# Optimization experiments

Measured on AMD Instinct MI355X. Metric: run time of the kernel, lower is better.

Reference implementation:

```python
import jax, jax.numpy as jnp
import numpy as np

H = W = 224
NSR = NSC = 8          # num_segments_row / col
BW = 5                 # band_width (default of adjust_boundaries)
K = NSR * NSC          # 64 superpixels
B = 256


def find_paths(g, inits, bw):
    """Seam-carving DP along axis 0 of g. g: (L, M); inits: (P,) start columns.
    Returns optimal paths (P, L) of column indices per row."""
    L, M = g.shape
    P = inits.shape[0]
    idx_pos = jnp.clip(inits[:, None] + jnp.arange(-bw, bw + 1)[None, :], 0, M - 1)  # (P, Np)
    Np = idx_pos.shape[1]
    C = -g[:, idx_pos]  # (L, P, Np) unary cost per row
    neigh = jnp.clip(jnp.arange(Np)[:, None] + jnp.array([-1, 0, 1])[None, :], 0, Np - 1)  # (Np,3)
    pos = jnp.arange(Np)
    r = jnp.arange(P)

    def step(cost_prev, c_y):
        padded = jnp.pad(cost_prev, ((0, 0), (1, 1)), constant_values=jnp.inf)  # (P, Np+2)
        prev_costs = padded[:, neigh + 1]                                        # (P, Np, 3)
        min_prev = prev_costs.min(axis=-1)
        min_idx = prev_costs.argmin(axis=-1)          # first-min, matches torch .min
        path_y = neigh[pos[None, :], min_idx]          # (P, Np) backpointers
        return min_prev + c_y, path_y

    cost_last, path_arr = jax.lax.scan(step, C[0], C[1:])  # path_arr: (L-1, P, Np)
    idx = jnp.argmin(cost_last, axis=1)                    # (P,)

    def back(idx, p_y):
        out = idx_pos[r, idx]
        return p_y[r, idx], out

    idx0, outs = jax.lax.scan(back, idx, path_arr, reverse=True)  # outs: (L-1, P) for y=1..L-1
    out0 = idx_pos[r, idx0]
    paths = jnp.concatenate([out0[None], outs], axis=0)  # (L, P)
    return paths.T


def segment_image(g):
    """g: (H, W) gradient map -> (H, W) int32 segmentation labels."""
    x_inits = jnp.clip(jnp.arange(1, NSC) * (W // NSC), 0, W - 1)
    y_inits = jnp.clip(jnp.arange(1, NSR) * (H // NSR), 0, H - 1)
    vpaths = find_paths(g, x_inits, BW)      # (7, H): column index per row
    hpaths = find_paths(g.T, y_inits, BW)    # (7, W): row index per column
    rows = jnp.broadcast_to(jnp.arange(H), vpaths.shape)
    cols = jnp.broadcast_to(jnp.arange(W), hpaths.shape)
    vmask = jnp.zeros((H, W), jnp.int32).at[rows, vpaths].set(1)
    hmask = jnp.zeros((H, W), jnp.int32).at[hpaths, cols].set(1)
    vlab = jnp.cumsum(vmask, axis=1)   # vertical label in [0, 7]
    hlab = jnp.cumsum(hmask, axis=0)   # horizontal label in [0, 7]
    return vlab + NSC * hlab           # labels in [0, 63]


def centroids_of(mask):
    flat = mask.reshape(-1)
    yc = jnp.repeat(jnp.arange(H, dtype=jnp.float32), W)
    xc = jnp.tile(jnp.arange(W, dtype=jnp.float32), H)
    sy = jax.ops.segment_sum(yc, flat, num_segments=K)
    sx = jax.ops.segment_sum(xc, flat, num_segments=K)
    cnt = jnp.maximum(jax.ops.segment_sum(jnp.ones_like(yc), flat, num_segments=K), 1e-6)
    return jnp.stack([sy / cnt, sx / cnt], axis=-1)  # (K, 2) [y, x]


def setup_inputs() -> dict:
    key = jax.random.key(0)
    k1, k2 = jax.random.split(key)
    x = jax.random.normal(k1, (B, 3, H, W), dtype=jnp.float32)
    grad_map = jax.random.uniform(k2, (B, H, W), dtype=jnp.float32)
    return {"x": x, "grad_map": grad_map}


def reference(x, grad_map):
    masks = jax.vmap(segment_image)(grad_map)          # (B, H, W) int32
    cents = jax.vmap(centroids_of)(masks)              # (B, K, 2) float32
    return cents, masks.astype(jnp.int64)
```

## Files before the change

kernel.cpp:

```cpp
#include <hip/hip_runtime.h>
#include <stdint.h>

#define HH 224
#define WW 224
#define NSEAM 7
#define BWIDTH 5
#define BB 256
#define KK 64
#define YCH 8
#define YROWS (HH / YCH)

#define DPPF_OLD(old, src, ctrl) \
    __int_as_float(__builtin_amdgcn_update_dpp(__float_as_int(old), __float_as_int(src), ctrl, 0xF, 0xF, false))
#define DPPF_Z(src, ctrl) \
    __int_as_float(__builtin_amdgcn_update_dpp(0, __float_as_int(src), ctrl, 0xF, 0xF, true))
#define DPPI_Z(src, ctrl) \
    __builtin_amdgcn_update_dpp(0, (int)(src), ctrl, 0xF, 0xF, true)

__global__ __launch_bounds__(256) void dp_kernel(const float* __restrict__ g,
                                                 int* __restrict__ paths,
                                                 unsigned long long* __restrict__ gacc) {
    __shared__ uint32_t ch[16][226];
    __shared__ int      pth[16][226];

    {
        int t = blockIdx.x * 256 + threadIdx.x;
        if (t < BB * KK) gacc[t] = 0ull;
    }

    const int j   = threadIdx.x & 15;
    const int grp = threadIdx.x >> 4;
    const int gid = blockIdx.x * 16 + grp;
    const int dir = gid / (BB * NSEAM);
    const int rem = gid - dir * (BB * NSEAM);
    const int b   = rem / NSEAM;
    const int p   = rem - b * NSEAM;
    const int band0 = 28 * (p + 1) - BWIDTH;
    const int jc  = (j > 10) ? 10 : j;
    const float* gb  = g + (size_t)b * HH * WW;
    const float* gp0 = gb + band0 + jc;
    const float* gp1 = gb + (size_t)(band0 + jc) * WW;
    const int shb  = threadIdx.x & 48;
    const int sel0 = (j == 0) ? 1 : 0;

    float bufA[16], bufB[16], cost;

#define LOADC(BUF, c)                                                       \
    if (dir == 0) {                                                         \
        _Pragma("unroll")                                                   \
        for (int rr = 0; rr < 16; ++rr) BUF[rr] = gp0[((c) * 16 + rr) * WW];\
    } else {                                                                \
        const float4* q4 = reinterpret_cast<const float4*>(gp1 + (c) * 16); \
        float4 t0 = q4[0], t1 = q4[1], t2 = q4[2], t3 = q4[3];              \
        BUF[0] = t0.x;  BUF[1] = t0.y;  BUF[2] = t0.z;  BUF[3] = t0.w;      \
        BUF[4] = t1.x;  BUF[5] = t1.y;  BUF[6] = t1.z;  BUF[7] = t1.w;      \
        BUF[8] = t2.x;  BUF[9] = t2.y;  BUF[10] = t2.z; BUF[11] = t2.w;     \
        BUF[12] = t3.x; BUF[13] = t3.y; BUF[14] = t3.z; BUF[15] = t3.w;     \
    }

#define ROWSTEP(BUF, rr, rbase)                                             \
    {                                                                       \
        float pm  = DPPF_OLD(cost, cost, 0x111);   \
        float ppv = DPPF_OLD(cost, cost, 0x101);  \
        ppv = (j >= 10) ? cost : ppv;                            \
        float best = fminf(fminf(pm, cost), ppv);                           \
        int sel = (pm == best) ? sel0 : ((cost == best) ? 1 : 2);           \
        cost = best - BUF[rr];                                              \
        unsigned long long b0 = __ballot(sel & 1);                          \
        unsigned long long b1 = __ballot(sel & 2);                          \
        if (j == 0) ch[grp][(rbase) + rr] =                                 \
            (uint32_t)(((b0 >> shb) & 0xFFFFull) |                          \
                       (((b1 >> shb) & 0xFFFFull) << 16));                  \
    }

#define PROCC(BUF, cbase)                                                   \
    _Pragma("unroll")                                                       \
    for (int rr = 0; rr < 16; ++rr) ROWSTEP(BUF, rr, (cbase) * 16)

    LOADC(bufA, 0);
    LOADC(bufB, 1);
    cost = -bufA[0];
#pragma unroll
    for (int rr = 1; rr < 16; ++rr) ROWSTEP(bufA, rr, 0);
    LOADC(bufA, 2);
    PROCC(bufB, 1);
    LOADC(bufB, 3);

#pragma unroll 1
    for (int c2 = 2; c2 <= 12; c2 += 2) {
        PROCC(bufA, c2);
        if (c2 + 2 < 14) LOADC(bufA, c2 + 2);
        PROCC(bufB, c2 + 1);
        if (c2 + 3 < 14) LOADC(bufB, c2 + 3);
    }

    float rc = (j <= 10) ? cost : INFINITY;
    int   ri = (j <= 10) ? j : 15;
#define REDSTEP(ctrl)                                                        \
    {                                                                        \
        float oc = DPPF_Z(rc, ctrl);                                         \
        int   oi = DPPI_Z(ri, ctrl);                                         \
        bool t = (oc < rc) || (oc == rc && oi < ri);                         \
        rc = t ? oc : rc; ri = t ? oi : ri;                                  \
    }
    REDSTEP(0x128) REDSTEP(0x124) REDSTEP(0x122) REDSTEP(0x121)
#undef REDSTEP

    int pos = ri;
    if (j == 0) pth[grp][HH - 1] = band0 + pos;

#pragma unroll 1
    for (int c = 13; c >= 0; --c) {
        uint32_t w[16];
#pragma unroll
        for (int rr = 0; rr < 16; ++rr) w[rr] = ch[grp][c * 16 + rr];
#pragma unroll
        for (int rr = 15; rr >= 0; --rr) {
            int r = c * 16 + rr;
            if (r >= 1) {
                uint32_t ww = w[rr];
                int sel = (int)((ww >> pos) & 1u) | (int)((ww >> (pos + 15)) & 2u);
                pos += sel - 1;
                if (j == 0) pth[grp][r - 1] = band0 + pos;
            }
        }
    }

    int* op = paths + (size_t)(b * 14 + dir * NSEAM + p) * HH;
#pragma unroll 1
    for (int c = 0; c < 14; ++c) op[c * 16 + j] = pth[grp][c * 16 + j];

#undef LOADC
#undef PROCC
#undef ROWSTEP
}

__global__ __launch_bounds__(256) void label_kernel(const int* __restrict__ paths,
                                                    float* __restrict__ out,
                                                    unsigned long long* __restrict__ gacc) {
    const int b  = blockIdx.x >> 3;
    const int cy = blockIdx.x & 7;
    const int y0 = cy * YROWS;

    __shared__ unsigned char vpc[NSEAM][YROWS];
    __shared__ unsigned long long acc[KK];

    const int* pb = paths + (size_t)b * 14 * HH;
    for (int i = threadIdx.x; i < NSEAM * YROWS; i += 256) {
        int q = i / YROWS, r = i - q * YROWS;
        vpc[q][r] = (unsigned char)pb[q * HH + y0 + r];
    }
    if (threadIdx.x < KK) acc[threadIdx.x] = 0ull;
    __syncthreads();

    const int x = threadIdx.x;
    if (x < WW) {
        int basev = 0, kv = 0, inv = 0;
        if (x >= 23) {
            int q = x - 23, k = q / 28, r = q - k * 28;
            if (k > 6) basev = 7;
            else { inv = (r <= 10) ? 1 : 0; basev = k + (r > 10 ? 1 : 0); kv = k; }
        }
        const int hA = (cy >= 1) ? pb[(NSEAM + cy - 1) * HH + x] : 0;
        const int hB = (cy <= 6) ? pb[(NSEAM + cy) * HH + x] : 0;

        float* mb = out + (size_t)BB * KK * 2 + (size_t)b * HH * WW + x;
        int cur = -1, ys = y0;

#define FLUSH(yend)                                                          \
        {                                                                    \
            unsigned cnt = (unsigned)((yend) - ys);                          \
            unsigned sy  = (unsigned)((ys + (yend) - 1) * ((yend) - ys) / 2);\
            unsigned sx  = (unsigned)x * cnt;                                \
            atomicAdd(&acc[cur], ((unsigned long long)cnt << 42) |           \
                                 ((unsigned long long)sy << 21) |            \
                                 (unsigned long long)sx);                    \
        }

#define ROW(t, HLEXPR)                                                       \
        {                                                                    \
            const int y = y0 + (t);                                          \
            int vl = basev + ((inv && (int)vpc[kv][t] <= x) ? 1 : 0);        \
            int lab = vl + 8 * (HLEXPR);                                     \
            mb[y * WW] = (float)lab;                                         \
            if (lab != cur) { if (cur >= 0) FLUSH(y); cur = lab; ys = y; }   \
        }

#pragma unroll
        for (int t = 0; t < 6; ++t)
            ROW(t, (cy >= 1) ? (cy - 1 + ((hA <= y0 + t) ? 1 : 0)) : 0)
#pragma unroll
        for (int t = 6; t < 23; ++t)
            ROW(t, cy)
#pragma unroll
        for (int t = 23; t < 28; ++t)
            ROW(t, (cy <= 6) ? (cy + ((hB <= y0 + t) ? 1 : 0)) : 7)

        FLUSH(y0 + YROWS)
#undef ROW
#undef FLUSH
    }
    __syncthreads();

    if (threadIdx.x < KK) {
        unsigned long long v = acc[threadIdx.x];
        if (v) atomicAdd(&gacc[(size_t)b * KK + threadIdx.x], v);
    }
}

__global__ __launch_bounds__(256) void finalize_kernel(const unsigned long long* __restrict__ gacc,
                                                       float* __restrict__ out) {
    int i = blockIdx.x * 256 + threadIdx.x;
    unsigned long long sv = gacc[i];
    float cnt = (float)(unsigned)(sv >> 42);
    float sy  = (float)(unsigned)((sv >> 21) & 0x1FFFFFu);
    float sx  = (float)(unsigned)(sv & 0x1FFFFFu);
    float c = fmaxf(cnt, 1e-6f);
    float2 r; r.x = sy / c; r.y = sx / c;
    *reinterpret_cast<float2*>(out + (size_t)i * 2) = r;
}

extern "C" void kernel_launch(void* const* d_in, const int* in_sizes, int n_in,
                              void* d_out, int out_size, void* d_ws, size_t ws_size,
                              hipStream_t stream) {
    const float* g = (const float*)d_in[1];
    float* out = (float*)d_out;
    int* paths = (int*)d_ws;
    unsigned long long* gacc =
        (unsigned long long*)((char*)d_ws + (size_t)BB * 14 * HH * 4);

    dp_kernel<<<(BB * 14) / 16, 256, 0, stream>>>(g, paths, gacc);
    label_kernel<<<BB * YCH, 256, 0, stream>>>(paths, out, gacc);
    finalize_kernel<<<(BB * KK) / 256, 256, 0, stream>>>(gacc, out);
}
```

Baseline: 47.02 us.

## Interleave vertical and horizontal seam DP chains within each thread group

Each 16-lane group now runs both the vertical and the horizontal seam DP for the same (image, seam) pair, with their row steps interleaved. The two chains are independent, so this adds instruction-level parallelism to a latency-bound serial scan. The DP grid drops to half as many blocks. In exchange it needs twice the shared memory, twice the load buffers and more registers per thread, and fewer CUs are occupied.

```diff
diff --git a/kernel.cpp b/kernel.cpp
--- a/kernel.cpp
+++ b/kernel.cpp
@@ -20,8 +20,8 @@
 __global__ __launch_bounds__(256) void dp_kernel(const float* __restrict__ g,
                                                  int* __restrict__ paths,
                                                  unsigned long long* __restrict__ gacc) {
-    __shared__ uint32_t ch[16][226];
-    __shared__ int      pth[16][226];
+    __shared__ uint32_t chA[16][226], chB[16][226];
+    __shared__ int      pthA[16][226], pthB[16][226];
 
     {
         int t = blockIdx.x * 256 + threadIdx.x;
@@ -30,11 +30,9 @@
 
     const int j   = threadIdx.x & 15;
     const int grp = threadIdx.x >> 4;
-    const int gid = blockIdx.x * 16 + grp;
-    const int dir = gid / (BB * NSEAM);
-    const int rem = gid - dir * (BB * NSEAM);
-    const int b   = rem / NSEAM;
-    const int p   = rem - b * NSEAM;
+    const int pi  = blockIdx.x * 16 + grp;
+    const int b   = pi / NSEAM;
+    const int p   = pi - b * NSEAM;
     const int band0 = 28 * (p + 1) - BWIDTH;
     const int jc  = (j > 10) ? 10 : j;
     const float* gb  = g + (size_t)b * HH * WW;
@@ -43,13 +41,15 @@
     const int shb  = threadIdx.x & 48;
     const int sel0 = (j == 0) ? 1 : 0;
 
-    float bufA[16], bufB[16], cost;
-
-#define LOADC(BUF, c)                                                       \
-    if (dir == 0) {                                                         \
-        _Pragma("unroll")                                                   \
-        for (int rr = 0; rr < 16; ++rr) BUF[rr] = gp0[((c) * 16 + rr) * WW];\
-    } else {                                                                \
+    float a0[16], a1[16], b0_[16], b1_[16];
+    float cost_a, cost_b;
+
+#define LOAD0(BUF, c)                                                       \
+    _Pragma("unroll")                                                       \
+    for (int rr = 0; rr < 16; ++rr) BUF[rr] = gp0[((c) * 16 + rr) * WW];
+
+#define LOAD1(BUF, c)                                                       \
+    {                                                                       \
         const float4* q4 = reinterpret_cast<const float4*>(gp1 + (c) * 16); \
         float4 t0 = q4[0], t1 = q4[1], t2 = q4[2], t3 = q4[3];              \
         BUF[0] = t0.x;  BUF[1] = t0.y;  BUF[2] = t0.z;  BUF[3] = t0.w;      \
@@ -58,81 +58,112 @@
         BUF[12] = t3.x; BUF[13] = t3.y; BUF[14] = t3.z; BUF[15] = t3.w;     \
     }
 
-#define ROWSTEP(BUF, rr, rbase)                                             \
+#define RS(BUF, rr, rbase, COST, CH)                                        \
     {                                                                       \
-        float pm  = DPPF_OLD(cost, cost, 0x111);   \
-        float ppv = DPPF_OLD(cost, cost, 0x101);  \
-        ppv = (j >= 10) ? cost : ppv;                            \
-        float best = fminf(fminf(pm, cost), ppv);                           \
-        int sel = (pm == best) ? sel0 : ((cost == best) ? 1 : 2);           \
-        cost = best - BUF[rr];                                              \
-        unsigned long long b0 = __ballot(sel & 1);                          \
-        unsigned long long b1 = __ballot(sel & 2);                          \
-        if (j == 0) ch[grp][(rbase) + rr] =                                 \
-            (uint32_t)(((b0 >> shb) & 0xFFFFull) |                          \
-                       (((b1 >> shb) & 0xFFFFull) << 16));                  \
-    }
-
-#define PROCC(BUF, cbase)                                                   \
+        float pm  = DPPF_OLD(COST, COST, 0x111);                            \
+        float ppv = DPPF_OLD(COST, COST, 0x101);                            \
+        ppv = (j >= 10) ? COST : ppv;                                       \
+        float best = fminf(fminf(pm, COST), ppv);                           \
+        int sel = (pm == best) ? sel0 : ((COST == best) ? 1 : 2);           \
+        COST = best - BUF[rr];                                              \
+        unsigned long long bb0 = __ballot(sel & 1);                         \
+        unsigned long long bb1 = __ballot(sel & 2);                         \
+        if (j == 0) CH[grp][(rbase) + rr] =                                 \
+            (uint32_t)(((bb0 >> shb) & 0xFFFFull) |                         \
+                       (((bb1 >> shb) & 0xFFFFull) << 16));                 \
+    }
+
+#define PROC2(BA, BBF, cbase)                                               \
     _Pragma("unroll")                                                       \
-    for (int rr = 0; rr < 16; ++rr) ROWSTEP(BUF, rr, (cbase) * 16)
-
-    LOADC(bufA, 0);
-    LOADC(bufB, 1);
-    cost = -bufA[0];
-#pragma unroll
-    for (int rr = 1; rr < 16; ++rr) ROWSTEP(bufA, rr, 0);
-    LOADC(bufA, 2);
-    PROCC(bufB, 1);
-    LOADC(bufB, 3);
+    for (int rr = 0; rr < 16; ++rr) {                                       \
+        RS(BA, rr, (cbase) * 16, cost_a, chA)                               \
+        RS(BBF, rr, (cbase) * 16, cost_b, chB)                              \
+    }
+
+    LOAD0(a0, 0);
+    LOAD1(b0_, 0);
+    LOAD0(a1, 1);
+    LOAD1(b1_, 1);
+    cost_a = -a0[0];
+    cost_b = -b0_[0];
+#pragma unroll
+    for (int rr = 1; rr < 16; ++rr) {
+        RS(a0, rr, 0, cost_a, chA)
+        RS(b0_, rr, 0, cost_b, chB)
+    }
+    LOAD0(a0, 2);
+    LOAD1(b0_, 2);
+    PROC2(a1, b1_, 1);
+    LOAD0(a1, 3);
+    LOAD1(b1_, 3);
 
 #pragma unroll 1
     for (int c2 = 2; c2 <= 12; c2 += 2) {
-        PROCC(bufA, c2);
-        if (c2 + 2 < 14) LOADC(bufA, c2 + 2);
-        PROCC(bufB, c2 + 1);
-        if (c2 + 3 < 14) LOADC(bufB, c2 + 3);
-    }
-
-    float rc = (j <= 10) ? cost : INFINITY;
-    int   ri = (j <= 10) ? j : 15;
+        PROC2(a0, b0_, c2);
+        if (c2 + 2 < 14) { LOAD0(a0, c2 + 2); LOAD1(b0_, c2 + 2); }
+        PROC2(a1, b1_, c2 + 1);
+        if (c2 + 3 < 14) { LOAD0(a1, c2 + 3); LOAD1(b1_, c2 + 3); }
+    }
+
+    float rcA = (j <= 10) ? cost_a : INFINITY;
+    int   riA = (j <= 10) ? j : 15;
+    float rcB = (j <= 10) ? cost_b : INFINITY;
+    int   riB = (j <= 10) ? j : 15;
 #define REDSTEP(ctrl)                                                        \
     {                                                                        \
-        float oc = DPPF_Z(rc, ctrl);                                         \
-        int   oi = DPPI_Z(ri, ctrl);                                         \
-        bool t = (oc < rc) || (oc == rc && oi < ri);                         \
-        rc = t ? oc : rc; ri = t ? oi : ri;                                  \
+        float oc = DPPF_Z(rcA, ctrl); int oi = DPPI_Z(riA, ctrl);            \
+        bool t = (oc < rcA) || (oc == rcA && oi < riA);                      \
+        rcA = t ? oc : rcA; riA = t ? oi : riA;                              \
+        float od = DPPF_Z(rcB, ctrl); int oj2 = DPPI_Z(riB, ctrl);           \
+        bool u = (od < rcB) || (od == rcB && oj2 < riB);                     \
+        rcB = u ? od : rcB; riB = u ? oj2 : riB;                             \
     }
     REDSTEP(0x128) REDSTEP(0x124) REDSTEP(0x122) REDSTEP(0x121)
 #undef REDSTEP
 
-    int pos = ri;
-    if (j == 0) pth[grp][HH - 1] = band0 + pos;
+    int posA = riA, posB = riB;
+    if (j == 0) {
+        pthA[grp][HH - 1] = band0 + posA;
+        pthB[grp][HH - 1] = band0 + posB;
+    }
 
 #pragma unroll 1
     for (int c = 13; c >= 0; --c) {
-        uint32_t w[16];
-#pragma unroll
-        for (int rr = 0; rr < 16; ++rr) w[rr] = ch[grp][c * 16 + rr];
+        uint32_t wA[16], wB[16];
+#pragma unroll
+        for (int rr = 0; rr < 16; ++rr) {
+            wA[rr] = chA[grp][c * 16 + rr];
+            wB[rr] = chB[grp][c * 16 + rr];
+        }
 #pragma unroll
         for (int rr = 15; rr >= 0; --rr) {
             int r = c * 16 + rr;
             if (r >= 1) {
-                uint32_t ww = w[rr];
-                int sel = (int)((ww >> pos) & 1u) | (int)((ww >> (pos + 15)) & 2u);
-                pos += sel - 1;
-                if (j == 0) pth[grp][r - 1] = band0 + pos;
+                uint32_t wa = wA[rr], wb = wB[rr];
+                int selA = (int)((wa >> posA) & 1u) | (int)((wa >> (posA + 15)) & 2u);
+                int selB = (int)((wb >> posB) & 1u) | (int)((wb >> (posB + 15)) & 2u);
+                posA += selA - 1;
+                posB += selB - 1;
+                if (j == 0) {
+                    pthA[grp][r - 1] = band0 + posA;
+                    pthB[grp][r - 1] = band0 + posB;
+                }
             }
         }
     }
 
-    int* op = paths + (size_t)(b * 14 + dir * NSEAM + p) * HH;
+    int* opA = paths + (size_t)(b * 14 + p) * HH;
+    int* opB = paths + (size_t)(b * 14 + NSEAM + p) * HH;
 #pragma unroll 1
-    for (int c = 0; c < 14; ++c) op[c * 16 + j] = pth[grp][c * 16 + j];
-
-#undef LOADC
-#undef PROCC
-#undef ROWSTEP
+    for (int c = 0; c < 14; ++c) {
+        opA[c * 16 + j] = pthA[grp][c * 16 + j];
+        opB[c * 16 + j] = pthB[grp][c * 16 + j];
+    }
+
+#undef LOAD0
+#undef LOAD1
+#undef RS
+#undef PROC2
 }
 
 __global__ __launch_bounds__(256) void label_kernel(const int* __restrict__ paths,
@@ -176,7 +207,6 @@
                                  ((unsigned long long)sy << 21) |            \
                                  (unsigned long long)sx);                    \
         }
-
 #define ROW(t, HLEXPR)                                                       \
         {                                                                    \
             const int y = y0 + (t);                                          \
@@ -185,7 +215,6 @@
             mb[y * WW] = (float)lab;                                         \
             if (lab != cur) { if (cur >= 0) FLUSH(y); cur = lab; ys = y; }   \
         }
-
 #pragma unroll
         for (int t = 0; t < 6; ++t)
             ROW(t, (cy >= 1) ? (cy - 1 + ((hA <= y0 + t) ? 1 : 0)) : 0)
@@ -195,7 +224,6 @@
 #pragma unroll
         for (int t = 23; t < 28; ++t)
             ROW(t, (cy <= 6) ? (cy + ((hB <= y0 + t) ? 1 : 0)) : 7)
-
         FLUSH(y0 + YROWS)
 #undef ROW
 #undef FLUSH
@@ -229,7 +257,7 @@
     unsigned long long* gacc =
         (unsigned long long*)((char*)d_ws + (size_t)BB * 14 * HH * 4);
 
-    dp_kernel<<<(BB * 14) / 16, 256, 0, stream>>>(g, paths, gacc);
+    dp_kernel<<<(BB * NSEAM) / 16, 256, 0, stream>>>(g, paths, gacc);
     label_kernel<<<BB * YCH, 256, 0, stream>>>(paths, out, gacc);
     finalize_kernel<<<(BB * KK) / 256, 256, 0, stream>>>(gacc, out);
 }
```

Result: slower. 68.06 us (+44.7%).

## Split DP into min-only forward chain and deferred backpointer selection pass

Applied to the files above, without the earlier changes.

The seam DP step now keeps only the min/subtract on the serial dependency chain and stores each row's cost into a 16-entry history register array. Backpointer selection, the two ballots and the shared-memory write are recomputed one chunk behind from the stored history, so they can interleave with the next chunk's forward chain. The aim is to shorten the latency-bound critical path. In exchange the DPP neighbour exchanges are done twice and register use goes up by 32 floats per thread.

```diff
diff --git a/kernel.cpp b/kernel.cpp
--- a/kernel.cpp
+++ b/kernel.cpp
@@ -43,7 +43,9 @@
     const int shb  = threadIdx.x & 48;
     const int sel0 = (j == 0) ? 1 : 0;
 
-    float bufA[16], bufB[16], cost;
+    float bufA[16], bufB[16];
+    float hE[16], hO[16];
+    float cost;
 
 #define LOADC(BUF, c)                                                       \
     if (dir == 0) {                                                         \
@@ -58,41 +60,61 @@
         BUF[12] = t3.x; BUF[13] = t3.y; BUF[14] = t3.z; BUF[15] = t3.w;     \
     }
 
-#define ROWSTEP(BUF, rr, rbase)                                             \
+#define FWDSTEP(BUF, HIST, rr)                                              \
     {                                                                       \
-        float pm  = DPPF_OLD(cost, cost, 0x111);   \
-        float ppv = DPPF_OLD(cost, cost, 0x101);  \
-        ppv = (j >= 10) ? cost : ppv;                            \
-        float best = fminf(fminf(pm, cost), ppv);                           \
-        int sel = (pm == best) ? sel0 : ((cost == best) ? 1 : 2);           \
-        cost = best - BUF[rr];                                              \
-        unsigned long long b0 = __ballot(sel & 1);                          \
-        unsigned long long b1 = __ballot(sel & 2);                          \
+        float pm  = DPPF_OLD(cost, cost, 0x111);                            \
+        float pv  = DPPF_OLD(cost, cost, 0x101);                            \
+        pv = (j >= 10) ? cost : pv;                                         \
+        cost = fminf(fminf(pm, cost), pv) - BUF[rr];                        \
+        HIST[rr] = cost;                                                    \
+    }
+
+#define FWDC(BUF, HIST)                                                     \
+    _Pragma("unroll")                                                       \
+    for (int rr = 0; rr < 16; ++rr) FWDSTEP(BUF, HIST, rr)
+
+#define SELSTEP(HIST, CARRY, rr, rbase)                                     \
+    {                                                                       \
+        float prev = (rr == 0) ? (CARRY) : HIST[(rr == 0) ? 0 : rr - 1];    \
+        float pm  = DPPF_OLD(prev, prev, 0x111);                            \
+        float pv  = DPPF_OLD(prev, prev, 0x101);                            \
+        pv = (j >= 10) ? prev : pv;                                         \
+        float best = fminf(fminf(pm, prev), pv);                            \
+        int sel = (pm == best) ? sel0 : ((prev == best) ? 1 : 2);           \
+        unsigned long long bb0 = __ballot(sel & 1);                         \
+        unsigned long long bb1 = __ballot(sel & 2);                         \
         if (j == 0) ch[grp][(rbase) + rr] =                                 \
-            (uint32_t)(((b0 >> shb) & 0xFFFFull) |                          \
-                       (((b1 >> shb) & 0xFFFFull) << 16));                  \
-    }
-
-#define PROCC(BUF, cbase)                                                   \
+            (uint32_t)(((bb0 >> shb) & 0xFFFFull) |                         \
+                       (((bb1 >> shb) & 0xFFFFull) << 16));                 \
+    }
+
+#define SELC(HIST, CARRY, cbase)                                            \
     _Pragma("unroll")                                                       \
-    for (int rr = 0; rr < 16; ++rr) ROWSTEP(BUF, rr, (cbase) * 16)
+    for (int rr = 0; rr < 16; ++rr) SELSTEP(HIST, CARRY, rr, (cbase) * 16)
 
     LOADC(bufA, 0);
     LOADC(bufB, 1);
     cost = -bufA[0];
-#pragma unroll
-    for (int rr = 1; rr < 16; ++rr) ROWSTEP(bufA, rr, 0);
+    hE[0] = cost;
+#pragma unroll
+    for (int rr = 1; rr < 16; ++rr) FWDSTEP(bufA, hE, rr);
     LOADC(bufA, 2);
-    PROCC(bufB, 1);
+    FWDC(bufB, hO);
+    SELC(hE, 0.0f, 0);
     LOADC(bufB, 3);
 
 #pragma unroll 1
     for (int c2 = 2; c2 <= 12; c2 += 2) {
-        PROCC(bufA, c2);
+        float carA = hE[15];
+        FWDC(bufA, hE);
+        SELC(hO, carA, c2 - 1);
+        float carB = hO[15];
         if (c2 + 2 < 14) LOADC(bufA, c2 + 2);
-        PROCC(bufB, c2 + 1);
+        FWDC(bufB, hO);
+        SELC(hE, carB, c2);
         if (c2 + 3 < 14) LOADC(bufB, c2 + 3);
     }
+    SELC(hO, hE[15], 13);
 
     float rc = (j <= 10) ? cost : INFINITY;
     int   ri = (j <= 10) ? j : 15;
@@ -131,8 +153,10 @@
     for (int c = 0; c < 14; ++c) op[c * 16 + j] = pth[grp][c * 16 + j];
 
 #undef LOADC
-#undef PROCC
-#undef ROWSTEP
+#undef FWDSTEP
+#undef FWDC
+#undef SELSTEP
+#undef SELC
 }
 
 __global__ __launch_bounds__(256) void label_kernel(const int* __restrict__ paths,
@@ -176,7 +200,6 @@
                                  ((unsigned long long)sy << 21) |            \
                                  (unsigned long long)sx);                    \
         }
-
 #define ROW(t, HLEXPR)                                                       \
         {                                                                    \
             const int y = y0 + (t);                                          \
@@ -185,7 +208,6 @@
             mb[y * WW] = (float)lab;                                         \
             if (lab != cur) { if (cur >= 0) FLUSH(y); cur = lab; ys = y; }   \
         }
-
 #pragma unroll
         for (int t = 0; t < 6; ++t)
             ROW(t, (cy >= 1) ? (cy - 1 + ((hA <= y0 + t) ? 1 : 0)) : 0)
@@ -195,7 +217,6 @@
 #pragma unroll
         for (int t = 23; t < 28; ++t)
             ROW(t, (cy <= 6) ? (cy + ((hB <= y0 + t) ? 1 : 0)) : 7)
-
         FLUSH(y0 + YROWS)
 #undef ROW
 #undef FLUSH
```

Result: slower. 50.26 us (+6.9%).
